# Kernel tuning notes

Hardware: AMD Instinct MI355X
Metric: run time of the kernel (lower is better)

## Reference

```python
import jax, jax.numpy as jnp
import numpy as np

B, T, D = 2, 1024, 1024
NUM_HEADS_ARG = 16
HS = D // NUM_HEADS_ARG          # 64 (per-head size)
H = HS                           # bug in source: num_heads passed = head_size -> 64 heads
FF = 4 * D
EPS = 1e-5


def _layernorm(x, gamma, beta):
    mu = jnp.mean(x, axis=-1, keepdims=True)
    var = jnp.mean(jnp.square(x - mu), axis=-1, keepdims=True)
    return (x - mu) * jax.lax.rsqrt(var + EPS) * gamma + beta


def setup_inputs() -> dict:
    key = jax.random.key(0)
    ks = jax.random.split(key, 12)
    s_d = 1.0 / np.sqrt(D)
    s_cat = 1.0 / np.sqrt(H * HS)
    s_ff = 1.0 / np.sqrt(FF)
    return {
        "x": jax.random.normal(ks[0], (B, T, D), jnp.float32),
        "Wq": jax.random.uniform(ks[1], (H, D, HS), jnp.float32, -s_d, s_d),
        "Wk": jax.random.uniform(ks[2], (H, D, HS), jnp.float32, -s_d, s_d),
        "Wv": jax.random.uniform(ks[3], (H, D, HS), jnp.float32, -s_d, s_d),
        "Wo": jax.random.uniform(ks[4], (H * HS, D), jnp.float32, -s_cat, s_cat),
        "bo": jax.random.uniform(ks[5], (D,), jnp.float32, -s_cat, s_cat),
        "W1": jax.random.uniform(ks[6], (D, FF), jnp.float32, -s_d, s_d),
        "b1": jax.random.uniform(ks[7], (FF,), jnp.float32, -s_d, s_d),
        "W2": jax.random.uniform(ks[8], (FF, D), jnp.float32, -s_ff, s_ff),
        "b2": jax.random.uniform(ks[9], (D,), jnp.float32, -s_ff, s_ff),
        "g1": jnp.ones((D,), jnp.float32),
        "be1": jnp.zeros((D,), jnp.float32),
        "g2": jnp.ones((D,), jnp.float32),
        "be2": jnp.zeros((D,), jnp.float32),
    }


def reference(x, Wq, Wk, Wv, Wo, bo, W1, b1, W2, b2, g1, be1, g2, be2):
    # per-head projections (no bias): [B,H,T,hs]
    q = jnp.einsum('btd,hde->bhte', x, Wq)
    k = jnp.einsum('btd,hde->bhte', x, Wk)
    v = jnp.einsum('btd,hde->bhte', x, Wv)
    scores = jnp.einsum('bhte,bhse->bhts', q, k) / np.sqrt(HS)  # [B,H,T,T]
    causal = jnp.tril(jnp.ones((T, T), bool))
    scores = jnp.where(causal, scores, -jnp.inf)
    probs = jax.nn.softmax(scores, axis=-1)
    att = jnp.einsum('bhts,bhse->bhte', probs, v)               # [B,H,T,hs]
    # torch stack(dim=3) -> [B,T,hs,H] then flatten: index = d*H + h
    cat = jnp.transpose(att, (0, 2, 3, 1)).reshape(B, T, HS * H)
    mha = cat @ Wo + bo
    x1 = _layernorm(x + mha, g1, be1)
    ff = jax.nn.relu(x1 @ W1 + b1) @ W2 + b2
    return _layernorm(x1 + ff, g2, be2)
```

## Files before the change

kernel.cpp:

```cpp
#include <hip/hip_runtime.h>

typedef unsigned short u16;
typedef __bf16 bf16x8 __attribute__((ext_vector_type(8)));
typedef float f32x4 __attribute__((ext_vector_type(4)));

#define B_ 2
#define T_ 1024
#define D_ 1024
#define H_ 64
#define HS_ 64
#define FF_ 4096
#define SZ_QKV 8388608L
#define S_SCALE 0.1803368801111f

__device__ __forceinline__ float bf2f(u16 u) {
  union { unsigned int v; float f; } x; x.v = ((unsigned int)u) << 16; return x.f;
}
__device__ __forceinline__ u16 f2bf(float f) {
  union { float f; unsigned int v; } x; x.f = f;
  unsigned int r = x.v + 0x7fffu + ((x.v >> 16) & 1u);
  return (u16)(r >> 16);
}
__device__ __forceinline__ u16 f2bf_rtz(float f) {
  union { float f; unsigned int v; } x; x.f = f;
  return (u16)(x.v >> 16);
}

typedef __attribute__((address_space(3))) unsigned int lds_u32;
typedef __attribute__((address_space(1))) const unsigned int glb_u32;
__device__ __forceinline__ void gload_lds16(const void* g, void* l) {
  __builtin_amdgcn_global_load_lds((glb_u32*)g, (lds_u32*)l, 16, 0, 0);
}

__global__ __launch_bounds__(256) void prep(
    const float* __restrict__ x, const float* __restrict__ Wq,
    const float* __restrict__ Wk, const float* __restrict__ Wv,
    const float* __restrict__ Wo, const float* __restrict__ W1,
    const float* __restrict__ W2,
    u16* __restrict__ xb, u16* __restrict__ Wqkvt, u16* __restrict__ Wot,
    u16* __restrict__ W1t, u16* __restrict__ W2t)
{
  __shared__ float tile[64][65];
  int id = blockIdx.x;
  if (id < 1024) {
    const long i = ((long)id * 256 + threadIdx.x) * 8;
    float4 a = *(const float4*)(x + i);
    float4 b = *(const float4*)(x + i + 4);
    union { uint4 v; u16 u[8]; } o;
    o.u[0]=f2bf(a.x); o.u[1]=f2bf(a.y); o.u[2]=f2bf(a.z); o.u[3]=f2bf(a.w);
    o.u[4]=f2bf(b.x); o.u[5]=f2bf(b.y); o.u[6]=f2bf(b.z); o.u[7]=f2bf(b.w);
    *(uint4*)(xb + i) = o.v;
    return;
  }
  id -= 1024;
  const float* in; u16* out; long ibase, obase; int in_rs, out_rs, r0, c0;
  if (id < 3072) {
    const int w = id >> 10, rem = id & 1023;
    const int z = rem >> 4, rt = rem & 15;
    in = (w == 0) ? Wq : (w == 1) ? Wk : Wv;
    ibase = (long)z * 65536; in_rs = 64; r0 = rt * 64; c0 = 0;
    out = Wqkvt + (long)w * 4194304;
    obase = (long)z * 65536; out_rs = 1024;
  } else if (id < 4096) {
    const int rem = id - 3072;
    const int z = rem >> 4, ct = rem & 15;
    in = Wo; ibase = (long)z * 1024; in_rs = 65536; r0 = 0; c0 = ct * 64;
    out = Wot; obase = (long)z * 64; out_rs = 4096;
  } else if (id < 5120) {
    const int rem = id - 4096;
    const int rt = rem >> 6, ct = rem & 63;
    in = W1; ibase = 0; in_rs = 4096; r0 = rt * 64; c0 = ct * 64;
    out = W1t; obase = 0; out_rs = 1024;
  } else {
    const int rem = id - 5120;
    const int rt = rem >> 4, ct = rem & 15;
    in = W2; ibase = 0; in_rs = 1024; r0 = rt * 64; c0 = ct * 64;
    out = W2t; obase = 0; out_rs = 4096;
  }
  const int t = threadIdx.x, lr = t >> 4, lc4 = (t & 15) * 4;
  #pragma unroll
  for (int j = 0; j < 4; ++j) {
    float4 f = *(const float4*)(in + ibase + (long)(r0 + lr + j * 16) * in_rs + c0 + lc4);
    tile[lr + j * 16][lc4]     = f.x;
    tile[lr + j * 16][lc4 + 1] = f.y;
    tile[lr + j * 16][lc4 + 2] = f.z;
    tile[lr + j * 16][lc4 + 3] = f.w;
  }
  __syncthreads();
  const int cr = t >> 3, ch = t & 7;
  #pragma unroll
  for (int j2 = 0; j2 < 2; ++j2) {
    const int crr = cr + j2 * 32;
    union { uint4 v; u16 u[8]; } o;
    #pragma unroll
    for (int i = 0; i < 8; ++i) o.u[i] = f2bf(tile[ch * 8 + i][crr]);
    *(uint4*)(out + obase + (long)(c0 + crr) * out_rs + r0 + ch * 8) = o.v;
  }
}

template<int TM, int EPI, int GRIDSWAP>
__global__ __launch_bounds__(256) void gemm_k(
    const u16* __restrict__ A, const u16* __restrict__ Bt, u16* __restrict__ C,
    const float* __restrict__ bias, int K, int lda, int ldb, int koff, int ldc)
{
  constexpr int NR = (TM == 128) ? 4 : 2;
  constexpr int AIT = TM / 64;
  __shared__ __attribute__((aligned(16))) u16 As[TM * 32];
  __shared__ __attribute__((aligned(16))) u16 Bs[128 * 32];
  __shared__ __attribute__((aligned(16))) u16 Es[4][16][72];
  const int bm = GRIDSWAP ? blockIdx.y : blockIdx.x;
  const int bn = GRIDSWAP ? blockIdx.x : blockIdx.y;
  const int bz = blockIdx.z;
  const long ko = (long)bz * koff;
  const int tid = threadIdx.x, wave = tid >> 6, lane = tid & 63;
  const int quad = lane >> 4, l16 = lane & 15;
  const int wm = (TM == 128) ? (wave & 1) * 64 : 0;
  const int wn = (TM == 128) ? (wave >> 1) * 64 : wave * 32;

  f32x4 acc[4][NR];
  #pragma unroll
  for (int i = 0; i < 4; ++i)
    #pragma unroll
    for (int j = 0; j < NR; ++j) acc[i][j] = (f32x4){0, 0, 0, 0};

  const int nK = K >> 5;
  for (int kc = 0; kc < nK; ++kc) {
    const int k0 = kc << 5;
    #pragma unroll
    for (int jA = 0; jA < AIT; ++jA) {
      const int i = jA * 4 + wave;
      const int chunk = i * 64 + lane;
      gload_lds16(A + (long)(bm * TM + (chunk >> 2)) * lda + ko + k0 + (chunk & 3) * 8,
                  (u16*)As + i * 512);
    }
    #pragma unroll
    for (int jB = 0; jB < 2; ++jB) {
      const int i = jB * 4 + wave;
      const int chunk = i * 64 + lane;
      gload_lds16(Bt + (long)(bn * 128 + (chunk >> 2)) * ldb + ko + k0 + (chunk & 3) * 8,
                  (u16*)Bs + i * 512);
    }
    __syncthreads();
    bf16x8 a[4], b[NR];
    #pragma unroll
    for (int i = 0; i < 4; ++i)
      a[i] = *(const bf16x8*)&As[(wm + i * 16 + l16) * 32 + quad * 8];
    #pragma unroll
    for (int j = 0; j < NR; ++j)
      b[j] = *(const bf16x8*)&Bs[(wn + j * 16 + l16) * 32 + quad * 8];
    #pragma unroll
    for (int i = 0; i < 4; ++i)
      #pragma unroll
      for (int j = 0; j < NR; ++j)
        acc[i][j] = __builtin_amdgcn_mfma_f32_16x16x32_bf16(a[i], b[j], acc[i][j], 0, 0, 0);
    __syncthreads();
  }

  if (EPI == 3) {
    #pragma unroll
    for (int j = 0; j < NR; ++j) {
      const int col = bn * 128 + wn + j * 16 + l16;
      #pragma unroll
      for (int i = 0; i < 4; ++i)
        #pragma unroll
        for (int r = 0; r < 4; ++r) {
          const int row = bm * TM + wm + i * 16 + quad * 4 + r;
          ((float*)C)[(long)bz * 2097152 + (long)row * ldc + col] = acc[i][j][r];
        }
    }
  } else {
    const int colbase = bn * 128 + wn;
    float bv[NR];
    #pragma unroll
    for (int j = 0; j < NR; ++j) bv[j] = (EPI == 1) ? bias[colbase + j * 16 + l16] : 0.f;
    const int rr = lane >> 2, ck = lane & 3;
    const int which = colbase >> 12, hh = (colbase >> 6) & 63;
    #pragma unroll
    for (int i = 0; i < 4; ++i) {
      #pragma unroll
      for (int j = 0; j < NR; ++j)
        #pragma unroll
        for (int r = 0; r < 4; ++r) {
          float vv = acc[i][j][r] + bv[j];
          if (EPI == 1) vv = fmaxf(vv, 0.f);
          Es[wave][quad * 4 + r][j * 16 + l16] = f2bf(vv);
        }
      const int row = bm * TM + wm + i * 16 + rr;
      uint4 w0 = *(const uint4*)&Es[wave][rr][ck * 8];
      uint4 w1 = *(const uint4*)&Es[wave][rr][32 + ck * 8];
      if (EPI == 2) {
        const int bb = row >> 10, tt = row & 1023;
        u16* dst = C + (long)which * SZ_QKV + ((long)(bb * 64 + hh)) * 65536L + tt * 64;
        *(uint4*)(dst + ck * 8) = w0;
        *(uint4*)(dst + 32 + ck * 8) = w1;
      } else {
        u16* dst = C + (long)row * ldc + colbase;
        *(uint4*)(dst + ck * 8) = w0;
        *(uint4*)(dst + 32 + ck * 8) = w1;
      }
    }
  }
}

__global__ __launch_bounds__(256) void attn_flash(
    const u16* __restrict__ Q, const u16* __restrict__ Kg,
    const u16* __restrict__ V, u16* __restrict__ Om)
{
  __shared__ __attribute__((aligned(16))) u16 Ks[2][64][72];
  __shared__ __attribute__((aligned(16))) u16 Vs[2][64][72];
  __shared__ __attribute__((aligned(16))) u16 QP[4][16][72];
  const int bh = blockIdx.x;
  const int qt = gridDim.y - 1 - blockIdx.y;
  const int b = bh >> 6, h = bh & 63;
  const long base = (long)bh * (T_ * HS_);
  const int tid = threadIdx.x;
  const int wave = tid >> 6, lane = tid & 63, quad = lane >> 4, l16 = lane & 15;
  const int sm = tid >> 2, sc = (tid & 3) * 16;
  const int vswz = (sc >> 4) << 3;

  {
    const int qr = lane >> 3, qe = (lane & 7) * 8;
    #pragma unroll
    for (int j = 0; j < 2; ++j) {
      union { uint4 v; u16 u[8]; } a, o;
      a.v = *(const uint4*)(Q + base + (long)(qt * 64 + wave * 16 + qr + j * 8) * HS_ + qe);
      #pragma unroll
      for (int i = 0; i < 8; ++i) o.u[i] = f2bf(bf2f(a.u[i]) * S_SCALE);
      *(uint4*)&QP[wave][qr + j * 8][qe] = o.v;
    }
  }
  bf16x8 aq0 = *(const bf16x8*)&QP[wave][l16][quad * 8];
  bf16x8 aq1 = *(const bf16x8*)&QP[wave][l16][32 + quad * 8];

  float psum[4] = { 0.f, 0.f, 0.f, 0.f };
  f32x4 oacc[4] = { {0,0,0,0}, {0,0,0,0}, {0,0,0,0}, {0,0,0,0} };

  uint4 kA, kB, vA, vB;
  kA = *(const uint4*)(Kg + base + (long)sm * HS_ + sc);
  kB = *(const uint4*)(Kg + base + (long)sm * HS_ + sc + 8);
  vA = *(const uint4*)(V  + base + (long)sm * HS_ + sc);
  vB = *(const uint4*)(V  + base + (long)sm * HS_ + sc + 8);
  {
    *(uint4*)&Ks[0][sm][sc] = kA; *(uint4*)&Ks[0][sm][sc + 8] = kB;
    union { uint4 v; u16 u[8]; } t0, t1; t0.v = vA; t1.v = vB;
    #pragma unroll
    for (int i = 0; i < 8; ++i) Vs[0][sc + i][sm ^ vswz] = t0.u[i];
    #pragma unroll
    for (int i = 0; i < 8; ++i) Vs[0][sc + 8 + i][sm ^ vswz] = t1.u[i];
  }
  __syncthreads();

  for (int kt = 0; kt <= qt; ++kt) {
    const int cur = kt & 1;
    const bool pf = (kt < qt);
    if (pf) {
      const long nb = base + (long)((kt + 1) * 64 + sm) * HS_ + sc;
      kA = *(const uint4*)(Kg + nb); kB = *(const uint4*)(Kg + nb + 8);
      vA = *(const uint4*)(V  + nb); vB = *(const uint4*)(V  + nb + 8);
    }

    f32x4 sacc[4] = { {0,0,0,0}, {0,0,0,0}, {0,0,0,0}, {0,0,0,0} };
    #pragma unroll
    for (int nt = 0; nt < 4; ++nt) {
      bf16x8 b0 = *(const bf16x8*)&Ks[cur][nt * 16 + l16][quad * 8];
      bf16x8 b1 = *(const bf16x8*)&Ks[cur][nt * 16 + l16][32 + quad * 8];
      sacc[nt] = __builtin_amdgcn_mfma_f32_16x16x32_bf16(aq0, b0, sacc[nt], 0, 0, 0);
      sacc[nt] = __builtin_amdgcn_mfma_f32_16x16x32_bf16(aq1, b1, sacc[nt], 0, 0, 0);
    }

    if (kt == qt) {
      #pragma unroll
      for (int nt = 0; nt < 4; ++nt) {
        const int col = nt * 16 + l16;
        #pragma unroll
        for (int r = 0; r < 4; ++r) {
          const int row = wave * 16 + quad * 4 + r;
          float p = exp2f(sacc[nt][r]);
          p = (col <= row) ? p : 0.f;
          sacc[nt][r] = p; psum[r] += p;
        }
      }
    } else {
      #pragma unroll
      for (int nt = 0; nt < 4; ++nt)
        #pragma unroll
        for (int r = 0; r < 4; ++r) {
          const float p = exp2f(sacc[nt][r]);
          sacc[nt][r] = p; psum[r] += p;
        }
    }

    #pragma unroll
    for (int nt = 0; nt < 4; ++nt)
      #pragma unroll
      for (int r = 0; r < 4; ++r)
        QP[wave][quad * 4 + r][nt * 16 + l16] = f2bf_rtz(sacc[nt][r]);
    bf16x8 p0 = *(const bf16x8*)&QP[wave][l16][quad * 8];
    bf16x8 p1 = *(const bf16x8*)&QP[wave][l16][32 + quad * 8];

    #pragma unroll
    for (int et = 0; et < 4; ++et) {
      const int c0 = ((quad ^ et) * 8);
      bf16x8 b0 = *(const bf16x8*)&Vs[cur][et * 16 + l16][c0];
      bf16x8 b1 = *(const bf16x8*)&Vs[cur][et * 16 + l16][32 + c0];
      oacc[et] = __builtin_amdgcn_mfma_f32_16x16x32_bf16(p0, b0, oacc[et], 0, 0, 0);
      oacc[et] = __builtin_amdgcn_mfma_f32_16x16x32_bf16(p1, b1, oacc[et], 0, 0, 0);
    }

    if (pf) {
      const int nxt = 1 - cur;
      *(uint4*)&Ks[nxt][sm][sc] = kA; *(uint4*)&Ks[nxt][sm][sc + 8] = kB;
      union { uint4 v; u16 u[8]; } t0, t1; t0.v = vA; t1.v = vB;
      #pragma unroll
      for (int i = 0; i < 8; ++i) Vs[nxt][sc + i][sm ^ vswz] = t0.u[i];
      #pragma unroll
      for (int i = 0; i < 8; ++i) Vs[nxt][sc + 8 + i][sm ^ vswz] = t1.u[i];
    }
    __syncthreads();
  }

  #pragma unroll
  for (int off = 1; off < 16; off <<= 1)
    #pragma unroll
    for (int r = 0; r < 4; ++r)
      psum[r] += __shfl_xor(psum[r], off, 64);
  u16 (*Os)[72] = Ks[0];
  #pragma unroll
  for (int r = 0; r < 4; ++r) {
    const float rinv = 1.f / fmaxf(psum[r], 1e-20f);
    const int row = wave * 16 + quad * 4 + r;
    #pragma unroll
    for (int et = 0; et < 4; ++et)
      Os[row][et * 16 + l16] = f2bf(oacc[et][r] * rinv);
  }
  const int orow = wave * 16 + (lane >> 3), oe = (lane & 7) * 8;
  #pragma unroll
  for (int it = 0; it < 2; ++it) {
    const int rr = orow + it * 8;
    uint4 o = *(const uint4*)&Os[rr][oe];
    *(uint4*)(Om + ((long)(b * T_ + qt * 64 + rr)) * 4096 + h * 64 + oe) = o;
  }
}

template<int XBF, int OBF>
__global__ __launch_bounds__(256) void ln_sum4(
    const float* __restrict__ P4, const float* __restrict__ bias,
    const void* __restrict__ Xv, const float* __restrict__ g,
    const float* __restrict__ be, void* __restrict__ outv)
{
  __shared__ float red[8];
  const int row = blockIdx.x, tid = threadIdx.x;
  const long base = (long)row * D_;
  float v4[4]; float s = 0.f;
  #pragma unroll
  for (int j = 0; j < 4; ++j) {
    const int i = tid + j * 256;
    float acc = bias[i];
    #pragma unroll
    for (int p = 0; p < 4; ++p) acc += P4[(long)p * 2097152 + base + i];
    const float xval = XBF ? bf2f(((const u16*)Xv)[base + i]) : ((const float*)Xv)[base + i];
    v4[j] = xval + acc;
    s += v4[j];
  }
  #pragma unroll
  for (int off = 32; off > 0; off >>= 1) s += __shfl_down(s, off, 64);
  if ((tid & 63) == 0) red[tid >> 6] = s;
  __syncthreads();
  const float mu = (red[0] + red[1] + red[2] + red[3]) * (1.f / D_);
  float vs = 0.f;
  #pragma unroll
  for (int j = 0; j < 4; ++j) { const float d = v4[j] - mu; vs += d * d; }
  #pragma unroll
  for (int off = 32; off > 0; off >>= 1) vs += __shfl_down(vs, off, 64);
  __syncthreads();
  if ((tid & 63) == 0) red[tid >> 6] = vs;
  __syncthreads();
  const float rs = rsqrtf((red[0] + red[1] + red[2] + red[3]) * (1.f / D_) + 1e-5f);
  #pragma unroll
  for (int j = 0; j < 4; ++j) {
    const int i = tid + j * 256;
    const float o = (v4[j] - mu) * rs * g[i] + be[i];
    if (OBF) ((u16*)outv)[base + i] = f2bf(o);
    else     ((float*)outv)[base + i] = o;
  }
}

extern "C" void kernel_launch(void* const* d_in, const int* in_sizes, int n_in,
                              void* d_out, int out_size, void* d_ws, size_t ws_size,
                              hipStream_t stream) {
  const float* x   = (const float*)d_in[0];
  const float* Wq  = (const float*)d_in[1];
  const float* Wk  = (const float*)d_in[2];
  const float* Wv  = (const float*)d_in[3];
  const float* Wo  = (const float*)d_in[4];
  const float* bo  = (const float*)d_in[5];
  const float* W1  = (const float*)d_in[6];
  const float* b1  = (const float*)d_in[7];
  const float* W2  = (const float*)d_in[8];
  const float* b2  = (const float*)d_in[9];
  const float* g1  = (const float*)d_in[10];
  const float* be1 = (const float*)d_in[11];
  const float* g2  = (const float*)d_in[12];
  const float* be2 = (const float*)d_in[13];
  float* out = (float*)d_out;

  u16* ws = (u16*)d_ws;
  u16* xb    = ws;
  u16* Wqkvt = xb + 2097152;
  u16* Wot   = Wqkvt + 12582912;
  u16* W1t   = Wot + 4194304;
  u16* W2t   = W1t + 4194304;
  u16* q     = W2t + 4194304;
  u16* k     = q + SZ_QKV;
  u16* v     = k + SZ_QKV;
  u16* Om    = v + SZ_QKV;
  float* P1 = (float*)q;
  float* P2 = (float*)q;
  u16* x1  = v;
  u16* h1  = Om;

  dim3 blk(256);

  prep<<<dim3(7168), blk, 0, stream>>>(x, Wq, Wk, Wv, Wo, W1, W2,
                                       xb, Wqkvt, Wot, W1t, W2t);

  gemm_k<128, 2, 1><<<dim3(96, 16), blk, 0, stream>>>(
      xb, Wqkvt, q, nullptr, 1024, 1024, 1024, 0, 0);

  attn_flash<<<dim3(128, 16), blk, 0, stream>>>(q, k, v, Om);

  gemm_k<64, 3, 0><<<dim3(32, 8, 4), blk, 0, stream>>>(
      Om, Wot, (u16*)P1, nullptr, 1024, 4096, 4096, 1024, 1024);

  ln_sum4<0, 1><<<dim3(2048), blk, 0, stream>>>(P1, bo, x, g1, be1, x1);

  gemm_k<128, 1, 1><<<dim3(32, 16), blk, 0, stream>>>(
      x1, W1t, h1, b1, 1024, 1024, 1024, 0, 4096);

  gemm_k<64, 3, 0><<<dim3(32, 8, 4), blk, 0, stream>>>(
      h1, W2t, (u16*)P2, nullptr, 1024, 4096, 4096, 1024, 1024);

  ln_sum4<1, 0><<<dim3(2048), blk, 0, stream>>>(P2, b2, x1, g2, be2, out);

  (void)in_sizes; (void)n_in; (void)out_size; (void)ws_size;
}
```

Before: 386.5 us.

## Process two 64-row query tiles per attention block to reuse K/V loads

Each attention workgroup now handles 128 query rows (two 64-row tiles) instead of 64, so every K/V tile staged in shared memory feeds MFMAs for both query tiles. The grid is halved along the query dimension and the lower tile skips its final diagonal step. This cuts global K/V traffic and LDS staging per unit of work, at the cost of more registers per wave, fewer blocks to spread across CUs, and more uneven causal load per block.

Result: slower. 541.8 us (+40.2%).

```diff
diff --git a/kernel.cpp b/kernel.cpp
--- a/kernel.cpp
+++ b/kernel.cpp
@@ -208,9 +208,9 @@
 {
   __shared__ __attribute__((aligned(16))) u16 Ks[2][64][72];
   __shared__ __attribute__((aligned(16))) u16 Vs[2][64][72];
-  __shared__ __attribute__((aligned(16))) u16 QP[4][16][72];
+  __shared__ __attribute__((aligned(16))) u16 QP[4][32][72];
   const int bh = blockIdx.x;
-  const int qt = gridDim.y - 1 - blockIdx.y;
+  const int bq = gridDim.y - 1 - blockIdx.y;
   const int b = bh >> 6, h = bh & 63;
   const long base = (long)bh * (T_ * HS_);
   const int tid = threadIdx.x;
@@ -221,20 +221,33 @@
   {
     const int qr = lane >> 3, qe = (lane & 7) * 8;
     #pragma unroll
-    for (int j = 0; j < 2; ++j) {
-      union { uint4 v; u16 u[8]; } a, o;
-      a.v = *(const uint4*)(Q + base + (long)(qt * 64 + wave * 16 + qr + j * 8) * HS_ + qe);
-      #pragma unroll
-      for (int i = 0; i < 8; ++i) o.u[i] = f2bf(bf2f(a.u[i]) * S_SCALE);
-      *(uint4*)&QP[wave][qr + j * 8][qe] = o.v;
-    }
-  }
-  bf16x8 aq0 = *(const bf16x8*)&QP[wave][l16][quad * 8];
-  bf16x8 aq1 = *(const bf16x8*)&QP[wave][l16][32 + quad * 8];
-
-  float psum[4] = { 0.f, 0.f, 0.f, 0.f };
-  f32x4 oacc[4] = { {0,0,0,0}, {0,0,0,0}, {0,0,0,0}, {0,0,0,0} };
-
+    for (int t = 0; t < 2; ++t)
+      #pragma unroll
+      for (int j = 0; j < 2; ++j) {
+        const int rit = qr + j * 8;
+        const long grow = (long)(bq * 128 + t * 64 + wave * 16 + rit);
+        union { uint4 v; u16 u[8]; } a, o;
+        a.v = *(const uint4*)(Q + base + grow * HS_ + qe);
+        #pragma unroll
+        for (int i = 0; i < 8; ++i) o.u[i] = f2bf(bf2f(a.u[i]) * S_SCALE);
+        *(uint4*)&QP[wave][t * 16 + rit][qe] = o.v;
+      }
+  }
+  bf16x8 aq[2][2];
+  #pragma unroll
+  for (int t = 0; t < 2; ++t)
+    #pragma unroll
+    for (int kk = 0; kk < 2; ++kk)
+      aq[t][kk] = *(const bf16x8*)&QP[wave][t * 16 + l16][kk * 32 + quad * 8];
+
+  float psum[2][4] = { {0,0,0,0}, {0,0,0,0} };
+  f32x4 oacc[2][4];
+  #pragma unroll
+  for (int t = 0; t < 2; ++t)
+    #pragma unroll
+    for (int et = 0; et < 4; ++et) oacc[t][et] = (f32x4){0,0,0,0};
+
+  const int qt_hi = 2 * bq + 1;
   uint4 kA, kB, vA, vB;
   kA = *(const uint4*)(Kg + base + (long)sm * HS_ + sc);
   kB = *(const uint4*)(Kg + base + (long)sm * HS_ + sc + 8);
@@ -250,61 +263,76 @@
   }
   __syncthreads();
 
-  for (int kt = 0; kt <= qt; ++kt) {
+  for (int kt = 0; kt <= qt_hi; ++kt) {
     const int cur = kt & 1;
-    const bool pf = (kt < qt);
+    const bool pf = (kt < qt_hi);
+    const bool t0a = pf;
+    const bool diag1 = (kt == qt_hi);
+    const bool diag0 = (kt == qt_hi - 1);
     if (pf) {
       const long nb = base + (long)((kt + 1) * 64 + sm) * HS_ + sc;
       kA = *(const uint4*)(Kg + nb); kB = *(const uint4*)(Kg + nb + 8);
       vA = *(const uint4*)(V  + nb); vB = *(const uint4*)(V  + nb + 8);
     }
 
-    f32x4 sacc[4] = { {0,0,0,0}, {0,0,0,0}, {0,0,0,0}, {0,0,0,0} };
+    f32x4 s0[4], s1[4];
+    #pragma unroll
+    for (int nt = 0; nt < 4; ++nt) { s0[nt] = (f32x4){0,0,0,0}; s1[nt] = (f32x4){0,0,0,0}; }
+    #pragma unroll
+    for (int kk = 0; kk < 2; ++kk) {
+      bf16x8 kf[4];
+      #pragma unroll
+      for (int nt = 0; nt < 4; ++nt)
+        kf[nt] = *(const bf16x8*)&Ks[cur][nt * 16 + l16][kk * 32 + quad * 8];
+      #pragma unroll
+      for (int nt = 0; nt < 4; ++nt) {
+        s1[nt] = __builtin_amdgcn_mfma_f32_16x16x32_bf16(aq[1][kk], kf[nt], s1[nt], 0, 0, 0);
+        if (t0a)
+          s0[nt] = __builtin_amdgcn_mfma_f32_16x16x32_bf16(aq[0][kk], kf[nt], s0[nt], 0, 0, 0);
+      }
+    }
+
     #pragma unroll
     for (int nt = 0; nt < 4; ++nt) {
-      bf16x8 b0 = *(const bf16x8*)&Ks[cur][nt * 16 + l16][quad * 8];
-      bf16x8 b1 = *(const bf16x8*)&Ks[cur][nt * 16 + l16][32 + quad * 8];
-      sacc[nt] = __builtin_amdgcn_mfma_f32_16x16x32_bf16(aq0, b0, sacc[nt], 0, 0, 0);
-      sacc[nt] = __builtin_amdgcn_mfma_f32_16x16x32_bf16(aq1, b1, sacc[nt], 0, 0, 0);
-    }
-
-    if (kt == qt) {
-      #pragma unroll
-      for (int nt = 0; nt < 4; ++nt) {
-        const int col = nt * 16 + l16;
-        #pragma unroll
-        for (int r = 0; r < 4; ++r) {
-          const int row = wave * 16 + quad * 4 + r;
-          float p = exp2f(sacc[nt][r]);
-          p = (col <= row) ? p : 0.f;
-          sacc[nt][r] = p; psum[r] += p;
+      const int col = nt * 16 + l16;
+      #pragma unroll
+      for (int r = 0; r < 4; ++r) {
+        const int row = wave * 16 + quad * 4 + r;
+        float p1 = exp2f(s1[nt][r]);
+        if (diag1) p1 = (col <= row) ? p1 : 0.f;
+        s1[nt][r] = p1; psum[1][r] += p1;
+        if (t0a) {
+          float p0 = exp2f(s0[nt][r]);
+          if (diag0) p0 = (col <= row) ? p0 : 0.f;
+          s0[nt][r] = p0; psum[0][r] += p0;
         }
       }
-    } else {
-      #pragma unroll
-      for (int nt = 0; nt < 4; ++nt)
-        #pragma unroll
-        for (int r = 0; r < 4; ++r) {
-          const float p = exp2f(sacc[nt][r]);
-          sacc[nt][r] = p; psum[r] += p;
-        }
     }
 
     #pragma unroll
     for (int nt = 0; nt < 4; ++nt)
       #pragma unroll
-      for (int r = 0; r < 4; ++r)
-        QP[wave][quad * 4 + r][nt * 16 + l16] = f2bf_rtz(sacc[nt][r]);
-    bf16x8 p0 = *(const bf16x8*)&QP[wave][l16][quad * 8];
-    bf16x8 p1 = *(const bf16x8*)&QP[wave][l16][32 + quad * 8];
-
-    #pragma unroll
-    for (int et = 0; et < 4; ++et) {
-      const int c0 = ((quad ^ et) * 8);
-      bf16x8 b0 = *(const bf16x8*)&Vs[cur][et * 16 + l16][c0];
-      bf16x8 b1 = *(const bf16x8*)&Vs[cur][et * 16 + l16][32 + c0];
-      oacc[et] = __builtin_amdgcn_mfma_f32_16x16x32_bf16(p0, b0, oacc[et], 0, 0, 0);
-      oacc[et] = __builtin_amdgcn_mfma_f32_16x16x32_bf16(p1, b1, oacc[et], 0, 0, 0);
+      for (int r = 0; r < 4; ++r) {
+        QP[wave][16 + quad * 4 + r][nt * 16 + l16] = f2bf_rtz(s1[nt][r]);
+        if (t0a) QP[wave][quad * 4 + r][nt * 16 + l16] = f2bf_rtz(s0[nt][r]);
+      }
+    bf16x8 p0[2], p1[2];
+    #pragma unroll
+    for (int kk = 0; kk < 2; ++kk) {
+      p1[kk] = *(const bf16x8*)&QP[wave][16 + l16][kk * 32 + quad * 8];
+      if (t0a) p0[kk] = *(const bf16x8*)&QP[wave][l16][kk * 32 + quad * 8];
+    }
+
+    #pragma unroll
+    for (int kk = 0; kk < 2; ++kk) {
+      #pragma unroll
+      for (int et = 0; et < 4; ++et) {
+        const int c0 = ((quad ^ et) * 8) + kk * 32;
+        bf16x8 vf = *(const bf16x8*)&Vs[cur][et * 16 + l16][c0];
+        oacc[1][et] = __builtin_amdgcn_mfma_f32_16x16x32_bf16(p1[kk], vf, oacc[1][et], 0, 0, 0);
+        if (t0a)
+          oacc[0][et] = __builtin_amdgcn_mfma_f32_16x16x32_bf16(p0[kk], vf, oacc[0][et], 0, 0, 0);
+      }
     }
 
     if (pf) {
@@ -322,23 +350,28 @@
   #pragma unroll
   for (int off = 1; off < 16; off <<= 1)
     #pragma unroll
-    for (int r = 0; r < 4; ++r)
-      psum[r] += __shfl_xor(psum[r], off, 64);
-  u16 (*Os)[72] = Ks[0];
-  #pragma unroll
-  for (int r = 0; r < 4; ++r) {
-    const float rinv = 1.f / fmaxf(psum[r], 1e-20f);
-    const int row = wave * 16 + quad * 4 + r;
-    #pragma unroll
-    for (int et = 0; et < 4; ++et)
-      Os[row][et * 16 + l16] = f2bf(oacc[et][r] * rinv);
-  }
-  const int orow = wave * 16 + (lane >> 3), oe = (lane & 7) * 8;
-  #pragma unroll
-  for (int it = 0; it < 2; ++it) {
-    const int rr = orow + it * 8;
-    uint4 o = *(const uint4*)&Os[rr][oe];
-    *(uint4*)(Om + ((long)(b * T_ + qt * 64 + rr)) * 4096 + h * 64 + oe) = o;
+    for (int t = 0; t < 2; ++t)
+      #pragma unroll
+      for (int r = 0; r < 4; ++r)
+        psum[t][r] += __shfl_xor(psum[t][r], off, 64);
+  u16* Os = &Ks[0][0][0];
+  #pragma unroll
+  for (int t = 0; t < 2; ++t)
+    #pragma unroll
+    for (int r = 0; r < 4; ++r) {
+      const float rinv = 1.f / fmaxf(psum[t][r], 1e-20f);
+      const int r128 = t * 64 + wave * 16 + quad * 4 + r;
+      #pragma unroll
+      for (int et = 0; et < 4; ++et)
+        Os[r128 * 72 + et * 16 + l16] = f2bf(oacc[t][et][r] * rinv);
+    }
+  __syncthreads();
+  const int oe = (tid & 7) * 8;
+  #pragma unroll
+  for (int it = 0; it < 4; ++it) {
+    const int r128 = it * 32 + (tid >> 3);
+    uint4 o = *(const uint4*)&Os[r128 * 72 + oe];
+    *(uint4*)(Om + ((long)(b * T_ + bq * 128 + r128)) * 4096 + h * 64 + oe) = o;
   }
 }
 
@@ -427,7 +460,7 @@
   gemm_k<128, 2, 1><<<dim3(96, 16), blk, 0, stream>>>(
       xb, Wqkvt, q, nullptr, 1024, 1024, 1024, 0, 0);
 
-  attn_flash<<<dim3(128, 16), blk, 0, stream>>>(q, k, v, Om);
+  attn_flash<<<dim3(128, 8), blk, 0, stream>>>(q, k, v, Om);
 
   gemm_k<64, 3, 0><<<dim3(32, 8, 4), blk, 0, stream>>>(
       Om, Wot, (u16*)P1, nullptr, 1024, 4096, 4096, 1024, 1024);
```
